# Kernel optimization log

Hardware: AMD Instinct MI355X
Metric: run time of the kernel (lower is better)

The kernel has to match this reference:

```python
import jax, jax.numpy as jnp
import numpy as np

B, T, N, F, H = 16, 128, 256, 128, 128


def setup_inputs() -> dict:
    key = jax.random.key(0)
    ks = jax.random.split(key, 9)
    s_x = (2.0 / (F + H)) ** 0.5  # glorot-ish scale for input kernels
    s_m = (2.0 / (H + H)) ** 0.5
    return {
        "x": jax.random.normal(ks[0], (B, T, N, F), dtype=jnp.float32),
        "Wix": jax.random.normal(ks[1], (F, H), dtype=jnp.float32) * s_x,
        "Wim": jax.random.normal(ks[2], (H, H), dtype=jnp.float32) * s_m,
        "Wfx": jax.random.normal(ks[3], (F, H), dtype=jnp.float32) * s_x,
        "Wfm": jax.random.normal(ks[4], (H, H), dtype=jnp.float32) * s_m,
        "Wcx": jax.random.normal(ks[5], (F, H), dtype=jnp.float32) * s_x,
        "Wcm": jax.random.normal(ks[6], (H, H), dtype=jnp.float32) * s_m,
        "Wox": jax.random.normal(ks[7], (F, H), dtype=jnp.float32) * s_x,
        "Wom": jax.random.normal(ks[8], (H, H), dtype=jnp.float32) * s_m,
        "bi": jnp.zeros((1, H), dtype=jnp.float32),
        "bf": jnp.zeros((1, H), dtype=jnp.float32),
        "bc": jnp.zeros((1, H), dtype=jnp.float32),
        "bo": jnp.zeros((1, H), dtype=jnp.float32),
    }


def _gclstm(x, Wix, Wim, Wfx, Wfm, Wcx, Wcm, Wox, Wom, bi, bf, bc, bo):
    b_, t_, n_, f_ = x.shape
    h_ = Wix.shape[1]
    # Fuse the 4 input-side matmuls into one GEMM (order: i, f, o, c)
    Wx = jnp.concatenate([Wix, Wfx, Wox, Wcx], axis=1)   # [F, 4H]
    Wm = jnp.concatenate([Wim, Wfm, Wom, Wcm], axis=1)   # [H, 4H]
    bias = jnp.concatenate([bi, bf, bo, bc], axis=1)      # [1, 4H]
    # Precompute input projections for all timesteps: [T, B, N, 4H]
    xw = jnp.einsum('btnf,fg->tbng', x, Wx) + bias

    def step(carry, xw_t):
        h, c = carry
        z = xw_t + h @ Wm                 # [B, N, 4H]
        zi, zf, zo, zg = jnp.split(z, 4, axis=-1)
        i = jax.nn.sigmoid(zi)
        f = jax.nn.sigmoid(zf)
        o = jax.nn.sigmoid(zo)
        g = jnp.tanh(zg)
        c_new = f * c + i * g
        h_new = o * jnp.tanh(c_new)
        return (h_new, c_new), h_new

    init = (jnp.zeros((b_, n_, h_), x.dtype), jnp.zeros((b_, n_, h_), x.dtype))
    _, states = jax.lax.scan(step, init, xw)  # [T, B, N, H]
    # Original does K.reshape(K.stack(states), [B, T, N, H]) (a raw reshape)
    return states.reshape(b_, t_, n_, h_)


def reference(x, Wix, Wim, Wfx, Wfm, Wcx, Wcm, Wox, Wom, bi, bf, bc, bo):
    return _gclstm(x, Wix, Wim, Wfx, Wfm, Wcx, Wcm, Wox, Wom, bi, bf, bc, bo)
```

## Files before the change

### kernel.cpp

```cpp
#include <hip/hip_runtime.h>
#include <hip/hip_bf16.h>


typedef __bf16 bf16x8 __attribute__((ext_vector_type(8)));
typedef float f32x4 __attribute__((ext_vector_type(4)));

#define PITCH 136

__device__ __forceinline__ unsigned short f2bf(float f) {
  unsigned int u = __float_as_uint(f);
  u += 0x7FFFu + ((u >> 16) & 1u);
  return (unsigned short)(u >> 16);
}
__device__ __forceinline__ unsigned long long pack4(float4 v) {
  return (unsigned long long)f2bf(v.x) |
         ((unsigned long long)f2bf(v.y) << 16) |
         ((unsigned long long)f2bf(v.z) << 32) |
         ((unsigned long long)f2bf(v.w) << 48);
}
__device__ __forceinline__ float sigm(float v) {
  return __fdividef(1.f, 1.f + __expf(-v));
}
__device__ __forceinline__ float tanh_(float v) {
  return 2.f * __fdividef(1.f, 1.f + __expf(-2.f * v)) - 1.f;
}

__global__ __launch_bounds__(256) void pack_w(
    const float* __restrict__ Wim, const float* __restrict__ Wfm,
    const float* __restrict__ Wom, const float* __restrict__ Wcm,
    const float* __restrict__ Wix, const float* __restrict__ Wfx,
    const float* __restrict__ Wox, const float* __restrict__ Wcx,
    unsigned short* __restrict__ WT) {
  int i = blockIdx.x * 256 + threadIdx.x;
  int zc = i >> 8, k = i & 255;
  int g = zc >> 7, hcol = zc & 127;
  const float* Wm_ = (g == 0) ? Wim : (g == 1) ? Wfm : (g == 2) ? Wom : Wcm;
  const float* Wx_ = (g == 0) ? Wix : (g == 1) ? Wfx : (g == 2) ? Wox : Wcx;
  float v = (k < 128) ? Wm_[k * 128 + hcol] : Wx_[(k - 128) * 128 + hcol];
  WT[i] = f2bf(v);
}

__global__ __launch_bounds__(512, 2) void lstm_persist(
    const float* __restrict__ x,
    const unsigned short* __restrict__ WT,
    const float* __restrict__ b_i, const float* __restrict__ b_f,
    const float* __restrict__ b_o, const float* __restrict__ b_c,
    float* __restrict__ out) {
  __shared__ unsigned short hbuf[2][16 * PITCH];
  __shared__ unsigned short xbuf[2][16 * PITCH];

  const int tid = threadIdx.x;
  const int w = tid >> 6, l = tid & 63;
  const int lr = l & 15, lh = l >> 4;
  const int bb = blockIdx.x >> 4;
  const int n0 = (blockIdx.x & 15) << 4;
  const int hc = (w << 4) + lr;

  bf16x8 B[4][8];
#pragma unroll
  for (int g = 0; g < 4; ++g)
#pragma unroll
    for (int kk = 0; kk < 8; ++kk)
      B[g][kk] = *(const bf16x8*)(WT +
          (size_t)(((g * 8 + w) * 16 + lr)) * 256 + lh * 8 + kk * 32);

  const float biv = b_i[hc], bfv = b_f[hc], bov = b_o[hc], bcv = b_c[hc];

  const int xrow = tid >> 5, xcol = (tid & 31) << 2;
  *(unsigned long long*)(&hbuf[0][xrow * PITCH + xcol]) = 0ull;
  const float* xblk = x + ((size_t)bb * 128 * 256 + n0) * 128;
  {
    float4 x0 = *(const float4*)(xblk + tid * 4);
    *(unsigned long long*)(&xbuf[0][xrow * PITCH + xcol]) = pack4(x0);
  }
  float cr[4] = {0.f, 0.f, 0.f, 0.f};
  __syncthreads();

  for (int t = 0; t < 128; ++t) {
    const int cur = t & 1, nxt = cur ^ 1;

    const int tp = (t + 1 < 128) ? t + 1 : 127;
    float4 xp = *(const float4*)(xblk + (size_t)tp * 32768 + tid * 4);

    bf16x8 ah[4], ax[4];
#pragma unroll
    for (int kk = 0; kk < 4; ++kk) {
      ah[kk] = *(const bf16x8*)(&hbuf[cur][lr * PITCH + lh * 8 + kk * 32]);
      ax[kk] = *(const bf16x8*)(&xbuf[cur][lr * PITCH + lh * 8 + kk * 32]);
    }

    f32x4 acc[4];
#pragma unroll
    for (int g = 0; g < 4; ++g) {
      f32x4 a_ = {0.f, 0.f, 0.f, 0.f};
#pragma unroll
      for (int kk = 0; kk < 4; ++kk)
        a_ = __builtin_amdgcn_mfma_f32_16x16x32_bf16(ah[kk], B[g][kk], a_, 0, 0, 0);
#pragma unroll
      for (int kk = 0; kk < 4; ++kk)
        a_ = __builtin_amdgcn_mfma_f32_16x16x32_bf16(ax[kk], B[g][kk + 4], a_, 0, 0, 0);
      acc[g] = a_;
    }

    float* outt = out + ((size_t)(t * 16 + bb) * 256 + n0) * 128;
#pragma unroll
    for (int r = 0; r < 4; ++r) {
      const float iv = sigm(acc[0][r] + biv);
      const float fv = sigm(acc[1][r] + bfv);
      const float ov = sigm(acc[2][r] + bov);
      const float gv = tanh_(acc[3][r] + bcv);
      const float cn = fv * cr[r] + iv * gv;
      cr[r] = cn;
      const float hv = ov * tanh_(cn);
      const int row = lh * 4 + r;
      outt[row * 128 + hc] = hv;
      hbuf[nxt][row * PITCH + hc] = f2bf(hv);
    }

    *(unsigned long long*)(&xbuf[nxt][xrow * PITCH + xcol]) = pack4(xp);

    __syncthreads();
  }
}

extern "C" void kernel_launch(void* const* d_in, const int* in_sizes, int n_in,
                              void* d_out, int out_size, void* d_ws, size_t ws_size,
                              hipStream_t stream) {
  (void)in_sizes; (void)n_in; (void)out_size; (void)ws_size;
  const float* x   = (const float*)d_in[0];
  const float* Wix = (const float*)d_in[1];
  const float* Wim = (const float*)d_in[2];
  const float* Wfx = (const float*)d_in[3];
  const float* Wfm = (const float*)d_in[4];
  const float* Wcx = (const float*)d_in[5];
  const float* Wcm = (const float*)d_in[6];
  const float* Wox = (const float*)d_in[7];
  const float* Wom = (const float*)d_in[8];
  const float* bi  = (const float*)d_in[9];
  const float* bf  = (const float*)d_in[10];
  const float* bc  = (const float*)d_in[11];
  const float* bo  = (const float*)d_in[12];

  unsigned short* WT = (unsigned short*)d_ws;
  float* out = (float*)d_out;

  pack_w<<<512, 256, 0, stream>>>(Wim, Wfm, Wom, Wcm, Wix, Wfx, Wox, Wcx, WT);
  lstm_persist<<<256, 512, 0, stream>>>(x, WT, bi, bf, bo, bc, out);
}
```

Baseline: 640.8 us.

## Pre-convert x to bf16, load x fragments directly into registers, transpose MFMA output

A separate kernel converts x to bf16 into workspace, so the recurrent kernel reads x fragments straight from global memory into registers instead of staging them through a shared xbuf. The MFMA operands are swapped so each lane holds four consecutive hidden columns, which allows float4 output stores and 8-byte h writes to shared memory. Biases are folded into the accumulator init, the time loop is unrolled by two, and the barrier is replaced by a plain waitcnt plus s_barrier. The cost is an extra full pass over x (read fp32, write bf16) plus another launch.

Result: slower. 666.9 us (+4.1%).

```diff
diff --git a/kernel.cpp b/kernel.cpp
--- a/kernel.cpp
+++ b/kernel.cpp
@@ -11,12 +11,6 @@
   unsigned int u = __float_as_uint(f);
   u += 0x7FFFu + ((u >> 16) & 1u);
   return (unsigned short)(u >> 16);
-}
-__device__ __forceinline__ unsigned long long pack4(float4 v) {
-  return (unsigned long long)f2bf(v.x) |
-         ((unsigned long long)f2bf(v.y) << 16) |
-         ((unsigned long long)f2bf(v.z) << 32) |
-         ((unsigned long long)f2bf(v.w) << 48);
 }
 __device__ __forceinline__ float sigm(float v) {
   return __fdividef(1.f, 1.f + __expf(-v));
@@ -40,87 +34,117 @@
   WT[i] = f2bf(v);
 }
 
+__global__ __launch_bounds__(256) void xcvt(const float* __restrict__ x,
+                                            unsigned short* __restrict__ xbf) {
+  size_t i = ((size_t)blockIdx.x * 256 + threadIdx.x) * 8;
+  float4 a = *(const float4*)(x + i);
+  float4 b = *(const float4*)(x + i + 4);
+  union { unsigned short us[8]; bf16x8 v; } cv;
+  cv.us[0] = f2bf(a.x); cv.us[1] = f2bf(a.y);
+  cv.us[2] = f2bf(a.z); cv.us[3] = f2bf(a.w);
+  cv.us[4] = f2bf(b.x); cv.us[5] = f2bf(b.y);
+  cv.us[6] = f2bf(b.z); cv.us[7] = f2bf(b.w);
+  *(bf16x8*)(xbf + i) = cv.v;
+}
+
 __global__ __launch_bounds__(512, 2) void lstm_persist(
-    const float* __restrict__ x,
+    const unsigned short* __restrict__ xbf,
     const unsigned short* __restrict__ WT,
     const float* __restrict__ b_i, const float* __restrict__ b_f,
     const float* __restrict__ b_o, const float* __restrict__ b_c,
     float* __restrict__ out) {
   __shared__ unsigned short hbuf[2][16 * PITCH];
-  __shared__ unsigned short xbuf[2][16 * PITCH];
 
   const int tid = threadIdx.x;
   const int w = tid >> 6, l = tid & 63;
   const int lr = l & 15, lh = l >> 4;
   const int bb = blockIdx.x >> 4;
   const int n0 = (blockIdx.x & 15) << 4;
-  const int hc = (w << 4) + lr;
+  const int hc0 = (w << 4) + (lh << 2);
 
-  bf16x8 B[4][8];
+  bf16x8 Wf[4][8];
 #pragma unroll
   for (int g = 0; g < 4; ++g)
 #pragma unroll
     for (int kk = 0; kk < 8; ++kk)
-      B[g][kk] = *(const bf16x8*)(WT +
-          (size_t)(((g * 8 + w) * 16 + lr)) * 256 + lh * 8 + kk * 32);
+      Wf[g][kk] = *(const bf16x8*)(WT +
+          (size_t)((g * 8 + w) * 16 + lr) * 256 + lh * 8 + kk * 32);
 
-  const float biv = b_i[hc], bfv = b_f[hc], bov = b_o[hc], bcv = b_c[hc];
+  f32x4 binit[4];
+#pragma unroll
+  for (int r = 0; r < 4; ++r) {
+    binit[0][r] = b_i[hc0 + r];
+    binit[1][r] = b_f[hc0 + r];
+    binit[2][r] = b_o[hc0 + r];
+    binit[3][r] = b_c[hc0 + r];
+  }
 
-  const int xrow = tid >> 5, xcol = (tid & 31) << 2;
-  *(unsigned long long*)(&hbuf[0][xrow * PITCH + xcol]) = 0ull;
-  const float* xblk = x + ((size_t)bb * 128 * 256 + n0) * 128;
   {
-    float4 x0 = *(const float4*)(xblk + tid * 4);
-    *(unsigned long long*)(&xbuf[0][xrow * PITCH + xcol]) = pack4(x0);
+    const int zr = tid >> 5, zc = (tid & 31) << 2;
+    *(unsigned long long*)(&hbuf[0][zr * PITCH + zc]) = 0ull;
   }
+
+  const unsigned short* xlane =
+      xbf + ((size_t)(bb * 128) * 256 + n0 + lr) * 128 + lh * 8;
+
+  bf16x8 xA[4], xB[4];
+#pragma unroll
+  for (int kk = 0; kk < 4; ++kk) xA[kk] = *(const bf16x8*)(xlane + kk * 32);
+
   float cr[4] = {0.f, 0.f, 0.f, 0.f};
   __syncthreads();
 
-  for (int t = 0; t < 128; ++t) {
-    const int cur = t & 1, nxt = cur ^ 1;
+#define STEP(T, XC, XN)                                                        \
+  {                                                                            \
+    const int cur = (T) & 1, nxt = cur ^ 1;                                    \
+    const int tp = ((T) + 1 < 128) ? (T) + 1 : 127;                            \
+    _Pragma("unroll")                                                          \
+    for (int kk = 0; kk < 4; ++kk)                                             \
+      XN[kk] = *(const bf16x8*)(xlane + (size_t)tp * 32768 + kk * 32);         \
+    bf16x8 hf[4];                                                              \
+    _Pragma("unroll")                                                          \
+    for (int kk = 0; kk < 4; ++kk)                                             \
+      hf[kk] = *(const bf16x8*)(&hbuf[cur][lr * PITCH + lh * 8 + kk * 32]);    \
+    f32x4 acc[4];                                                              \
+    _Pragma("unroll")                                                          \
+    for (int g = 0; g < 4; ++g) {                                              \
+      f32x4 a_ = binit[g];                                                     \
+      _Pragma("unroll")                                                        \
+      for (int kk = 0; kk < 4; ++kk)                                           \
+        a_ = __builtin_amdgcn_mfma_f32_16x16x32_bf16(Wf[g][kk + 4], XC[kk],    \
+                                                     a_, 0, 0, 0);             \
+      _Pragma("unroll")                                                        \
+      for (int kk = 0; kk < 4; ++kk)                                           \
+        a_ = __builtin_amdgcn_mfma_f32_16x16x32_bf16(Wf[g][kk], hf[kk],        \
+                                                     a_, 0, 0, 0);             \
+      acc[g] = a_;                                                             \
+    }                                                                          \
+    float4 ov;                                                                 \
+    unsigned long long hp = 0ull;                                              \
+    _Pragma("unroll")                                                          \
+    for (int r = 0; r < 4; ++r) {                                              \
+      const float iv = sigm(acc[0][r]);                                        \
+      const float fv = sigm(acc[1][r]);                                        \
+      const float o_ = sigm(acc[2][r]);                                        \
+      const float gv = tanh_(acc[3][r]);                                       \
+      const float cn = fv * cr[r] + iv * gv;                                   \
+      cr[r] = cn;                                                              \
+      const float hv = o_ * tanh_(cn);                                         \
+      ((float*)&ov)[r] = hv;                                                   \
+      hp |= (unsigned long long)f2bf(hv) << (16 * r);                          \
+    }                                                                          \
+    *(float4*)(out + ((size_t)((T) * 16 + bb) * 256 + n0 + lr) * 128 + hc0) =  \
+        ov;                                                                    \
+    *(unsigned long long*)(&hbuf[nxt][lr * PITCH + hc0]) = hp;                 \
+    asm volatile("s_waitcnt lgkmcnt(0)\n\ts_barrier" ::: "memory");            \
+    __builtin_amdgcn_sched_barrier(0);                                         \
+  }
 
-    const int tp = (t + 1 < 128) ? t + 1 : 127;
-    float4 xp = *(const float4*)(xblk + (size_t)tp * 32768 + tid * 4);
-
-    bf16x8 ah[4], ax[4];
-#pragma unroll
-    for (int kk = 0; kk < 4; ++kk) {
-      ah[kk] = *(const bf16x8*)(&hbuf[cur][lr * PITCH + lh * 8 + kk * 32]);
-      ax[kk] = *(const bf16x8*)(&xbuf[cur][lr * PITCH + lh * 8 + kk * 32]);
-    }
-
-    f32x4 acc[4];
-#pragma unroll
-    for (int g = 0; g < 4; ++g) {
-      f32x4 a_ = {0.f, 0.f, 0.f, 0.f};
-#pragma unroll
-      for (int kk = 0; kk < 4; ++kk)
-        a_ = __builtin_amdgcn_mfma_f32_16x16x32_bf16(ah[kk], B[g][kk], a_, 0, 0, 0);
-#pragma unroll
-      for (int kk = 0; kk < 4; ++kk)
-        a_ = __builtin_amdgcn_mfma_f32_16x16x32_bf16(ax[kk], B[g][kk + 4], a_, 0, 0, 0);
-      acc[g] = a_;
-    }
-
-    float* outt = out + ((size_t)(t * 16 + bb) * 256 + n0) * 128;
-#pragma unroll
-    for (int r = 0; r < 4; ++r) {
-      const float iv = sigm(acc[0][r] + biv);
-      const float fv = sigm(acc[1][r] + bfv);
-      const float ov = sigm(acc[2][r] + bov);
-      const float gv = tanh_(acc[3][r] + bcv);
-      const float cn = fv * cr[r] + iv * gv;
-      cr[r] = cn;
-      const float hv = ov * tanh_(cn);
-      const int row = lh * 4 + r;
-      outt[row * 128 + hc] = hv;
-      hbuf[nxt][row * PITCH + hc] = f2bf(hv);
-    }
-
-    *(unsigned long long*)(&xbuf[nxt][xrow * PITCH + xcol]) = pack4(xp);
-
-    __syncthreads();
+  for (int t = 0; t < 128; t += 2) {
+    STEP(t, xA, xB)
+    STEP(t + 1, xB, xA)
   }
+#undef STEP
 }
 
 extern "C" void kernel_launch(void* const* d_in, const int* in_sizes, int n_in,
@@ -141,9 +165,12 @@
   const float* bc  = (const float*)d_in[11];
   const float* bo  = (const float*)d_in[12];
 
-  unsigned short* WT = (unsigned short*)d_ws;
+  char* ws = (char*)d_ws;
+  unsigned short* WT  = (unsigned short*)ws;
+  unsigned short* xbf = (unsigned short*)(ws + (1 << 20));
   float* out = (float*)d_out;
 
   pack_w<<<512, 256, 0, stream>>>(Wim, Wfm, Wom, Wcm, Wix, Wfx, Wox, Wcx, WT);
-  lstm_persist<<<256, 512, 0, stream>>>(x, WT, bi, bf, bo, bc, out);
+  xcvt<<<32768, 256, 0, stream>>>(x, xbf);
+  lstm_persist<<<256, 512, 0, stream>>>(xbf, WT, bi, bf, bo, bc, out);
 }
```
